# Kernel tuning notes

Measured on AMD Instinct MI355X. Metric: run time of the kernel, lower is better.

## Reference

```python
import jax, jax.numpy as jnp
import numpy as np

N_EMBEDDING = 32
HEAD_SIZE = 64
B, T = 8, 4096


def setup_inputs() -> dict:
    key = jax.random.key(0)
    kx, kk, kq, kv = jax.random.split(key, 4)
    x = jax.random.normal(kx, (B, T, N_EMBEDDING), dtype=jnp.float32)
    Wk = jax.random.normal(kk, (N_EMBEDDING, HEAD_SIZE), dtype=jnp.float32) * 0.05
    Wq = jax.random.normal(kq, (N_EMBEDDING, HEAD_SIZE), dtype=jnp.float32) * 0.05
    Wv = jax.random.normal(kv, (N_EMBEDDING, HEAD_SIZE), dtype=jnp.float32) * 0.05
    return {"x": x, "Wk": Wk, "Wq": Wq, "Wv": Wv}


def reference(x, Wk, Wq, Wv):
    # x: [B, T, C]; projections (no bias)
    k = jnp.einsum("btc,cd->btd", x, Wk)  # [B,T,D]
    q = jnp.einsum("btc,cd->btd", x, Wq)
    v = jnp.einsum("btc,cd->btd", x, Wv)
    # raw scores (NOTE: original module applies no 1/sqrt(D) scaling)
    wei = jnp.einsum("bqd,bkd->bqk", q, k)  # [B,T,T]
    t = x.shape[1]
    causal = jnp.tril(jnp.ones((t, t), dtype=bool))
    wei = jnp.where(causal[None, :, :], wei, -jnp.inf)
    wei = jax.nn.softmax(wei, axis=-1)
    out = jnp.einsum("bqk,bkd->bqd", wei, v)  # [B,T,D]
    return out
```

## Files before the change

kernel.cpp:

```cpp
#include <hip/hip_runtime.h>
#include <hip/hip_bf16.h>

constexpr int Bc = 8;
constexpr int Tt = 4096;
constexpr int Dd = 64;

typedef __attribute__((ext_vector_type(8))) short short8;
typedef __attribute__((ext_vector_type(4))) float floatx4;
typedef __attribute__((ext_vector_type(4))) __fp16 half4;
typedef __attribute__((ext_vector_type(2))) __fp16 half2v;
typedef uint4   __attribute__((may_alias)) uint4_a;
typedef short8  __attribute__((may_alias)) short8_a;
typedef ushort4 __attribute__((may_alias)) ushort4_a;
typedef float4  __attribute__((may_alias)) float4_a;
typedef half4   __attribute__((may_alias)) half4_a;

#define MFMA16(A, B, C)  __builtin_amdgcn_mfma_f32_16x16x32_bf16(A, B, C, 0, 0, 0)
#define MFMAH16(A, B, C) __builtin_amdgcn_mfma_f32_16x16x16f16(A, B, C, 0, 0, 0)
constexpr float LOG2E = 1.4426950408889634f;

__device__ __forceinline__ unsigned rnd16(float x) {
    unsigned u; __builtin_memcpy(&u, &x, 4); return u + 0x8000u;
}
__device__ __forceinline__ unsigned pk_bf2(float lo, float hi) {
    return __builtin_amdgcn_perm(rnd16(hi), rnd16(lo), 0x07060302);
}
__device__ __forceinline__ ushort4 pack4(floatx4 d) {
    union { unsigned u[2]; ushort4 v; } r;
    r.u[0] = pk_bf2(d[0], d[1]);
    r.u[1] = pk_bf2(d[2], d[3]);
    return r.v;
}
__device__ __forceinline__ short8 cvt8(float4 a, float4 b) {
    union { unsigned u[4]; short8 s; } r;
    r.u[0] = pk_bf2(a.x, a.y);
    r.u[1] = pk_bf2(a.z, a.w);
    r.u[2] = pk_bf2(b.x, b.y);
    r.u[3] = pk_bf2(b.z, b.w);
    return r.s;
}

__global__ __launch_bounds__(1024, 4) void attn_kernel(
    const float* __restrict__ x,
    const float* __restrict__ Wk, const float* __restrict__ Wq,
    const float* __restrict__ Wv,
    float* __restrict__ out)
{
    __shared__ uint4 sStage[4096];
    __shared__ uint4 sP[256];
    __shared__ uint4 sG[128];

    int b  = blockIdx.x & 7;
    int pr = blockIdx.x >> 3;
    int tid  = threadIdx.x;
    int wave = tid >> 6, lane = tid & 63;
    int group = wave >> 2, gw = wave & 3;
    int ln15 = lane & 15, quad = lane >> 4;
    size_t bT = (size_t)b * Tt;

    const int tg = tid & 255;
    const int srow = tg >> 2, scg = tg & 3;

    if (wave == 0) {
        floatx4 gC[2][2];
        #pragma unroll
        for (int mt = 0; mt < 2; ++mt)
            #pragma unroll
            for (int nt = 0; nt < 2; ++nt) gC[mt][nt] = (floatx4){0.f,0.f,0.f,0.f};
        #pragma unroll
        for (int kt = 0; kt < 2; ++kt) {
            short8 aG[2], bG[2];
            #pragma unroll
            for (int mt = 0; mt < 2; ++mt) {
                const float* qp = Wq + (ln15 + 16*mt)*64 + 32*kt + quad*8;
                float4 a = ((const float4_a*)qp)[0], bb = ((const float4_a*)qp)[1];
                a.x*=LOG2E; a.y*=LOG2E; a.z*=LOG2E; a.w*=LOG2E;
                bb.x*=LOG2E; bb.y*=LOG2E; bb.z*=LOG2E; bb.w*=LOG2E;
                aG[mt] = cvt8(a, bb);
                const float* kp = Wk + (ln15 + 16*mt)*64 + 32*kt + quad*8;
                bG[mt] = cvt8(((const float4_a*)kp)[0], ((const float4_a*)kp)[1]);
            }
            #pragma unroll
            for (int mt = 0; mt < 2; ++mt)
                #pragma unroll
                for (int nt = 0; nt < 2; ++nt)
                    gC[mt][nt] = MFMA16(aG[mt], bG[nt], gC[mt][nt]);
        }
        unsigned short* sGh = (unsigned short*)sG;
        #pragma unroll
        for (int mt = 0; mt < 2; ++mt)
            #pragma unroll
            for (int nt = 0; nt < 2; ++nt)
                *(ushort4_a*)(sGh + (16*nt + ln15)*32 + 16*mt + quad*4)
                    = pack4(gC[mt][nt]);
    }
    __syncthreads();

    const int gBase = group * 1024;
    unsigned short* sYh = (unsigned short*)sP;

    for (int phase = 0; phase < 2; ++phase) {
        const int qtP = phase ? pr : 63 - pr;
        const int q0 = qtP * 64;
        const int qrow = q0 + gw*16 + ln15;

        float4 pX0, pX1;
        if (group <= qtP) {
            const float* xp = x + (bT + group*64 + srow)*32 + scg*8;
            pX0 = ((const float4_a*)xp)[0];
            pX1 = ((const float4_a*)xp)[1];
        }

        if (wave < 8) {
            int qs = wave & 3, mt = wave >> 2;
            union { uint4 u; short8 s; } g;
            g.u = sG[(16*mt + ln15)*4 + quad];
            const float* xp = x + (bT + q0 + qs*16 + ln15)*32 + quad*8;
            short8 xq = cvt8(((const float4_a*)xp)[0], ((const float4_a*)xp)[1]);
            floatx4 d = (floatx4){0.f,0.f,0.f,0.f};
            d = MFMA16(g.s, xq, d);
            *(ushort4_a*)(sYh + (qs*16 + ln15)*32 + 16*mt + quad*4) = pack4(d);
        }
        __syncthreads();
        short8 bq;
        {
            union { uint4 u; short8 s; } t0;
            t0.u = sP[(gw*16 + ln15)*4 + quad];
            bq = t0.s;
        }

        floatx4 z4[2];
        z4[0] = (floatx4){0.f,0.f,0.f,0.f};
        z4[1] = (floatx4){0.f,0.f,0.f,0.f};
        float l_lane = 0.f;

        const int nIter = (qtP + 4) >> 2;

        for (int it = 0; it < nIter; ++it) {
            int kt = 4*it + group;
            bool active = (kt <= qtP);
            const int stB = gBase + (it & 1) * 512;
            if (active) {
                unsigned u0 = pk_bf2(pX0.x, pX0.y), u1 = pk_bf2(pX0.z, pX0.w);
                unsigned u2 = pk_bf2(pX1.x, pX1.y), u3 = pk_bf2(pX1.z, pX1.w);
                uint4 xu; xu.x = u0; xu.y = u1; xu.z = u2; xu.w = u3;
                sStage[stB + srow*4 + (scg ^ (srow & 3))] = xu;
                union { half2v h; unsigned short us[2]; } w01, w23, w45, w67;
                w01.h = __builtin_amdgcn_cvt_pkrtz(pX0.x, pX0.y);
                w23.h = __builtin_amdgcn_cvt_pkrtz(pX0.z, pX0.w);
                w45.h = __builtin_amdgcn_cvt_pkrtz(pX1.x, pX1.y);
                w67.h = __builtin_amdgcn_cvt_pkrtz(pX1.z, pX1.w);
                unsigned short hv[8] = { w01.us[0], w01.us[1], w23.us[0], w23.us[1],
                                         w45.us[0], w45.us[1], w67.us[0], w67.us[1] };
                unsigned short* sXh = (unsigned short*)(sStage + stB + 256);
                const int cb = scg * 8, gx = srow >> 2, ko = srow & 3;
                #pragma unroll
                for (int jj = 0; jj < 8; ++jj) {
                    int c = cb + jj;
                    sXh[c*64 + ((gx ^ (c & 15)) << 2) + ko] = hv[jj];
                }
            }
            __syncthreads();
            int ktn = kt + 4;
            if (ktn <= qtP) {
                const float* xp = x + (bT + ktn*64 + srow)*32 + scg*8;
                pX0 = ((const float4_a*)xp)[0];
                pX1 = ((const float4_a*)xp)[1];
            }
            if (!active) continue;
            int k0 = kt * 64;

            const int xsw = quad ^ (ln15 & 3);
            floatx4 s4[4];
            #pragma unroll
            for (int t = 0; t < 4; ++t) {
                union { uint4 u; short8 s; } a;
                a.u = sStage[stB + (16*t + ln15)*4 + xsw];
                floatx4 c = (floatx4){0.f,0.f,0.f,0.f};
                c = MFMA16(a.s, bq, c);
                s4[t] = c;
            }

            if (kt == qtP) {
                #pragma unroll
                for (int t = 0; t < 4; ++t) {
                    int keyb = k0 + 16*t + quad*4;
                    #pragma unroll
                    for (int r = 0; r < 4; ++r) {
                        float p = (keyb + r <= qrow) ? __builtin_amdgcn_exp2f(s4[t][r]) : 0.f;
                        s4[t][r] = p;
                        l_lane += p;
                    }
                }
            } else {
                #pragma unroll
                for (int t = 0; t < 4; ++t)
                    #pragma unroll
                    for (int r = 0; r < 4; ++r) {
                        float p = __builtin_amdgcn_exp2f(s4[t][r]);
                        s4[t][r] = p;
                        l_lane += p;
                    }
            }

            const unsigned short* sXh = (const unsigned short*)(sStage + stB + 256);
            #pragma unroll
            for (int t = 0; t < 4; ++t) {
                union { half2v h2[2]; half4 h4; } pb;
                pb.h2[0] = __builtin_amdgcn_cvt_pkrtz(s4[t][0], s4[t][1]);
                pb.h2[1] = __builtin_amdgcn_cvt_pkrtz(s4[t][2], s4[t][3]);
                const int gph = ((4*t + quad) ^ ln15) << 2;
                #pragma unroll
                for (int mt = 0; mt < 2; ++mt) {
                    half4 xa = *(const half4_a*)(sXh + (16*mt + ln15)*64 + gph);
                    z4[mt] = MFMAH16(xa, pb.h4, z4[mt]);
                }
            }
        }

        __syncthreads();
        int li = gw*64 + lane;
        ((float*)sP)[wave*64 + lane] = l_lane;
        if (group != 0) {
            float4* st = (float4*)(sStage + group*1024);
            st[li*2 + 0] = make_float4(z4[0][0], z4[0][1], z4[0][2], z4[0][3]);
            st[li*2 + 1] = make_float4(z4[1][0], z4[1][1], z4[1][2], z4[1][3]);
        }
        __syncthreads();
        if (group == 0) {
            short8 wv_f[4];
            #pragma unroll
            for (int t = 0; t < 4; ++t) {
                int col = 16*t + ln15;
                union { unsigned u[4]; short8 s; } rv;
                #pragma unroll
                for (int jj = 0; jj < 4; ++jj) {
                    const float* v0 = Wv + (quad*8 + 2*jj) * 64 + col;
                    rv.u[jj] = pk_bf2(v0[0], v0[64]);
                }
                wv_f[t] = rv.s;
            }
            float l = l_lane + ((float*)sP)[256 + li]
                    + ((float*)sP)[512 + li] + ((float*)sP)[768 + li];
            l += __shfl_xor(l, 16);
            l += __shfl_xor(l, 32);
            float inv = 1.f / l;
            #pragma unroll
            for (int g = 1; g < 4; ++g) {
                float4* st = (float4*)(sStage + g*1024);
                float4 a = st[li*2 + 0], bb = st[li*2 + 1];
                z4[0][0]+=a.x; z4[0][1]+=a.y; z4[0][2]+=a.z; z4[0][3]+=a.w;
                z4[1][0]+=bb.x; z4[1][1]+=bb.y; z4[1][2]+=bb.z; z4[1][3]+=bb.w;
            }
            unsigned short* sZb = (unsigned short*)sStage;
            #pragma unroll
            for (int mt = 0; mt < 2; ++mt)
                *(ushort4_a*)(sZb + (gw*16 + ln15)*32 + 16*mt + quad*4) = pack4(z4[mt]);
            union { uint4 u; short8 s; } zb;
            zb.u = sStage[(gw*16 + ln15)*4 + quad];
            #pragma unroll
            for (int t = 0; t < 4; ++t) {
                floatx4 o = (floatx4){0.f,0.f,0.f,0.f};
                o = MFMA16(wv_f[t], zb.s, o);
                *(float4_a*)(out + (bT + q0 + gw*16 + ln15)*Dd + 16*t + quad*4)
                    = make_float4(o[0]*inv, o[1]*inv, o[2]*inv, o[3]*inv);
            }
        }
        __syncthreads();
    }
}

extern "C" void kernel_launch(void* const* d_in, const int* in_sizes, int n_in,
                              void* d_out, int out_size, void* d_ws, size_t ws_size,
                              hipStream_t stream)
{
    const float* x  = (const float*)d_in[0];
    const float* Wk = (const float*)d_in[1];
    const float* Wq = (const float*)d_in[2];
    const float* Wv = (const float*)d_in[3];
    float* out = (float*)d_out;

    attn_kernel<<<Bc * 32, 1024, 0, stream>>>(x, Wk, Wq, Wv, out);
}
```

Measured before the change: 87.46 us.

## Split into prep kernel precomputing bf16/fp16 x layouts, then barrier-free attention

```diff
diff --git a/kernel.cpp b/kernel.cpp
--- a/kernel.cpp
+++ b/kernel.cpp
@@ -19,6 +19,11 @@
 #define MFMAH16(A, B, C) __builtin_amdgcn_mfma_f32_16x16x16f16(A, B, C, 0, 0, 0)
 constexpr float LOG2E = 1.4426950408889634f;
 
+constexpr size_t XB_OFF = 0;
+constexpr size_t YB_OFF = (size_t)2 << 20;
+constexpr size_t XT_OFF = (size_t)4 << 20;
+constexpr size_t WV_OFF = (size_t)6 << 20;
+
 __device__ __forceinline__ unsigned rnd16(float x) {
     unsigned u; __builtin_memcpy(&u, &x, 4); return u + 0x8000u;
 }
@@ -40,26 +45,29 @@
     return r.s;
 }
 
-__global__ __launch_bounds__(1024, 4) void attn_kernel(
+__global__ __launch_bounds__(256) void prep_kernel(
     const float* __restrict__ x,
     const float* __restrict__ Wk, const float* __restrict__ Wq,
     const float* __restrict__ Wv,
-    float* __restrict__ out)
+    char* __restrict__ ws)
 {
-    __shared__ uint4 sStage[4096];
-    __shared__ uint4 sP[256];
     __shared__ uint4 sG[128];
-
-    int b  = blockIdx.x & 7;
-    int pr = blockIdx.x >> 3;
-    int tid  = threadIdx.x;
-    int wave = tid >> 6, lane = tid & 63;
-    int group = wave >> 2, gw = wave & 3;
-    int ln15 = lane & 15, quad = lane >> 4;
-    size_t bT = (size_t)b * Tt;
-
-    const int tg = tid & 255;
-    const int srow = tg >> 2, scg = tg & 3;
+    __shared__ float sX[2048];
+
+    const int bi = blockIdx.x;
+    const int b = bi >> 6, ch = bi & 63;
+    const int tid = threadIdx.x;
+    const int wave = tid >> 6, lane = tid & 63;
+    const int ln15 = lane & 15, quad = lane >> 4;
+    const size_t bT = (size_t)b * Tt;
+    const int r0 = ch * 64;
+
+    const int lr = wave * 16 + ln15;
+    const float* xp = x + (bT + r0 + lr) * 32 + quad * 8;
+    float4 pX0 = ((const float4_a*)xp)[0];
+    float4 pX1 = ((const float4_a*)xp)[1];
+    *(float4_a*)(&sX[lr * 32 + quad * 8])     = pX0;
+    *(float4_a*)(&sX[lr * 32 + quad * 8 + 4]) = pX1;
 
     if (wave == 0) {
         floatx4 gC[2][2];
@@ -96,36 +104,85 @@
     }
     __syncthreads();
 
-    const int gBase = group * 1024;
-    unsigned short* sYh = (unsigned short*)sP;
-
-    for (int phase = 0; phase < 2; ++phase) {
-        const int qtP = phase ? pr : 63 - pr;
-        const int q0 = qtP * 64;
-        const int qrow = q0 + gw*16 + ln15;
-
-        float4 pX0, pX1;
-        if (group <= qtP) {
-            const float* xp = x + (bT + group*64 + srow)*32 + scg*8;
-            pX0 = ((const float4_a*)xp)[0];
-            pX1 = ((const float4_a*)xp)[1];
-        }
-
-        if (wave < 8) {
-            int qs = wave & 3, mt = wave >> 2;
+    union { unsigned u[4]; uint4 v; } xu;
+    xu.u[0] = pk_bf2(pX0.x, pX0.y); xu.u[1] = pk_bf2(pX0.z, pX0.w);
+    xu.u[2] = pk_bf2(pX1.x, pX1.y); xu.u[3] = pk_bf2(pX1.z, pX1.w);
+    *(uint4_a*)(ws + XB_OFF + (size_t)(bT + r0 + lr) * 64 + quad * 16) = xu.v;
+
+    {
+        short8 xq = cvt8(pX0, pX1);
+        unsigned short* yb = (unsigned short*)(ws + YB_OFF);
+        #pragma unroll
+        for (int mt = 0; mt < 2; ++mt) {
             union { uint4 u; short8 s; } g;
             g.u = sG[(16*mt + ln15)*4 + quad];
-            const float* xp = x + (bT + q0 + qs*16 + ln15)*32 + quad*8;
-            short8 xq = cvt8(((const float4_a*)xp)[0], ((const float4_a*)xp)[1]);
             floatx4 d = (floatx4){0.f,0.f,0.f,0.f};
             d = MFMA16(g.s, xq, d);
-            *(ushort4_a*)(sYh + (qs*16 + ln15)*32 + 16*mt + quad*4) = pack4(d);
-        }
-        __syncthreads();
+            *(ushort4_a*)(yb + (size_t)(bT + r0 + lr) * 32 + 16*mt + quad*4)
+                = pack4(d);
+        }
+    }
+
+    {
+        const int kc = tid >> 6;
+        const int c = (tid >> 1) & 31, kh = tid & 1;
+        float v[8];
+        #pragma unroll
+        for (int j = 0; j < 8; ++j) v[j] = sX[(kc*16 + kh*8 + j)*32 + c];
+        union { unsigned u[4]; uint4 q; } x4;
+        #pragma unroll
+        for (int j = 0; j < 4; ++j) {
+            union { half2v h; unsigned u; } p;
+            p.h = __builtin_amdgcn_cvt_pkrtz(v[2*j], v[2*j+1]);
+            x4.u[j] = p.u;
+        }
+        *(uint4_a*)(ws + XT_OFF
+                    + ((size_t)((b*256 + ch*4 + kc) * 32 + c)) * 32 + kh * 16)
+            = x4.q;
+    }
+
+    if (bi == 0 && wave == 2) {
+        const int d = lane;
+        unsigned short* wvb = (unsigned short*)(ws + WV_OFF);
+        float v[32];
+        #pragma unroll
+        for (int c2 = 0; c2 < 32; ++c2) v[c2] = Wv[c2*64 + d];
+        #pragma unroll
+        for (int i2 = 0; i2 < 16; ++i2)
+            ((unsigned*)(wvb + d*32))[i2] = pk_bf2(v[2*i2], v[2*i2+1]);
+    }
+}
+
+__global__ __launch_bounds__(1024, 4) void attn_kernel(
+    const char* __restrict__ ws, float* __restrict__ out)
+{
+    __shared__ float sZ[3 * 2048];
+    __shared__ float sL[3 * 256];
+    __shared__ uint4 sB[256];
+
+    const int b  = blockIdx.x & 7;
+    const int pr = blockIdx.x >> 3;
+    const int tid = threadIdx.x;
+    const int wave = tid >> 6, lane = tid & 63;
+    const int kg = wave >> 2, gw = wave & 3;
+    const int ln15 = lane & 15, quad = lane >> 4;
+    const size_t bT = (size_t)b * Tt;
+
+    const char* xbB = ws + XB_OFF + bT * 64;
+    const char* xtB = ws + XT_OFF + (size_t)b * (256 * 1024);
+    const int aOff = ln15 * 64 + quad * 16;
+    const int xOff = ln15 * 32 + quad * 8;
+
+    for (int phase = 0; phase < 2; ++phase) {
+        const int qt = phase ? pr : 63 - pr;
+        const int q0 = qt * 64;
+        const int qrow = q0 + gw * 16 + ln15;
+
         short8 bq;
         {
             union { uint4 u; short8 s; } t0;
-            t0.u = sP[(gw*16 + ln15)*4 + quad];
+            t0.u = *(const uint4_a*)(ws + YB_OFF + (size_t)(bT + qrow) * 64
+                                     + quad * 16);
             bq = t0.s;
         }
 
@@ -134,62 +191,38 @@
         z4[1] = (floatx4){0.f,0.f,0.f,0.f};
         float l_lane = 0.f;
 
-        const int nIter = (qtP + 4) >> 2;
-
-        for (int it = 0; it < nIter; ++it) {
-            int kt = 4*it + group;
-            bool active = (kt <= qtP);
-            const int stB = gBase + (it & 1) * 512;
-            if (active) {
-                unsigned u0 = pk_bf2(pX0.x, pX0.y), u1 = pk_bf2(pX0.z, pX0.w);
-                unsigned u2 = pk_bf2(pX1.x, pX1.y), u3 = pk_bf2(pX1.z, pX1.w);
-                uint4 xu; xu.x = u0; xu.y = u1; xu.z = u2; xu.w = u3;
-                sStage[stB + srow*4 + (scg ^ (srow & 3))] = xu;
-                union { half2v h; unsigned short us[2]; } w01, w23, w45, w67;
-                w01.h = __builtin_amdgcn_cvt_pkrtz(pX0.x, pX0.y);
-                w23.h = __builtin_amdgcn_cvt_pkrtz(pX0.z, pX0.w);
-                w45.h = __builtin_amdgcn_cvt_pkrtz(pX1.x, pX1.y);
-                w67.h = __builtin_amdgcn_cvt_pkrtz(pX1.z, pX1.w);
-                unsigned short hv[8] = { w01.us[0], w01.us[1], w23.us[0], w23.us[1],
-                                         w45.us[0], w45.us[1], w67.us[0], w67.us[1] };
-                unsigned short* sXh = (unsigned short*)(sStage + stB + 256);
-                const int cb = scg * 8, gx = srow >> 2, ko = srow & 3;
-                #pragma unroll
-                for (int jj = 0; jj < 8; ++jj) {
-                    int c = cb + jj;
-                    sXh[c*64 + ((gx ^ (c & 15)) << 2) + ko] = hv[jj];
-                }
-            }
-            __syncthreads();
-            int ktn = kt + 4;
-            if (ktn <= qtP) {
-                const float* xp = x + (bT + ktn*64 + srow)*32 + scg*8;
-                pX0 = ((const float4_a*)xp)[0];
-                pX1 = ((const float4_a*)xp)[1];
-            }
-            if (!active) continue;
-            int k0 = kt * 64;
-
-            const int xsw = quad ^ (ln15 & 3);
+        short8 aA[4], aB4[4];
+
+        auto LDA = [&](int k, short8* a) {
+            const char* p = xbB + (size_t)k * 4096 + aOff;
+            #pragma unroll
+            for (int t = 0; t < 4; ++t)
+                a[t] = *(const short8_a*)(p + t * 1024);
+        };
+
+        auto BODY = [&](int kt, const short8* a) {
+            const char* px = xtB + (size_t)kt * 4096 + xOff;
+            half4 xa[8];
+            #pragma unroll
+            for (int t = 0; t < 4; ++t) {
+                xa[2*t]   = *(const half4_a*)(px + t * 1024);
+                xa[2*t+1] = *(const half4_a*)(px + t * 1024 + 512);
+            }
             floatx4 s4[4];
             #pragma unroll
             for (int t = 0; t < 4; ++t) {
-                union { uint4 u; short8 s; } a;
-                a.u = sStage[stB + (16*t + ln15)*4 + xsw];
-                floatx4 c = (floatx4){0.f,0.f,0.f,0.f};
-                c = MFMA16(a.s, bq, c);
-                s4[t] = c;
-            }
-
-            if (kt == qtP) {
+                floatx4 c0 = (floatx4){0.f,0.f,0.f,0.f};
+                s4[t] = MFMA16(a[t], bq, c0);
+            }
+            if (kt == qt) {
                 #pragma unroll
                 for (int t = 0; t < 4; ++t) {
-                    int keyb = k0 + 16*t + quad*4;
+                    const int keyb = kt*64 + 16*t + quad*4;
                     #pragma unroll
                     for (int r = 0; r < 4; ++r) {
-                        float p = (keyb + r <= qrow) ? __builtin_amdgcn_exp2f(s4[t][r]) : 0.f;
-                        s4[t][r] = p;
-                        l_lane += p;
+                        float p = (keyb + r <= qrow)
+                                  ? __builtin_amdgcn_exp2f(s4[t][r]) : 0.f;
+                        s4[t][r] = p; l_lane += p;
                     }
                 }
             } else {
@@ -198,71 +231,76 @@
                     #pragma unroll
                     for (int r = 0; r < 4; ++r) {
                         float p = __builtin_amdgcn_exp2f(s4[t][r]);
-                        s4[t][r] = p;
-                        l_lane += p;
+                        s4[t][r] = p; l_lane += p;
                     }
             }
-
-            const unsigned short* sXh = (const unsigned short*)(sStage + stB + 256);
             #pragma unroll
             for (int t = 0; t < 4; ++t) {
                 union { half2v h2[2]; half4 h4; } pb;
                 pb.h2[0] = __builtin_amdgcn_cvt_pkrtz(s4[t][0], s4[t][1]);
                 pb.h2[1] = __builtin_amdgcn_cvt_pkrtz(s4[t][2], s4[t][3]);
-                const int gph = ((4*t + quad) ^ ln15) << 2;
-                #pragma unroll
-                for (int mt = 0; mt < 2; ++mt) {
-                    half4 xa = *(const half4_a*)(sXh + (16*mt + ln15)*64 + gph);
-                    z4[mt] = MFMAH16(xa, pb.h4, z4[mt]);
-                }
+                z4[0] = MFMAH16(xa[2*t],   pb.h4, z4[0]);
+                z4[1] = MFMAH16(xa[2*t+1], pb.h4, z4[1]);
+            }
+        };
+
+        int kt = kg;
+        if (kt <= qt) {
+            LDA(kt, aA);
+            while (true) {
+                int kn = kt + 4;
+                LDA(kn <= qt ? kn : kt, aB4);
+                BODY(kt, aA);
+                if (kn > qt) break;
+                kt = kn; kn = kt + 4;
+                LDA(kn <= qt ? kn : kt, aA);
+                BODY(kt, aB4);
+                if (kn > qt) break;
+                kt = kn;
             }
         }
 
         __syncthreads();
-        int li = gw*64 + lane;
-        ((float*)sP)[wave*64 + lane] = l_lane;
-        if (group != 0) {
-            float4* st = (float4*)(sStage + group*1024);
-            st[li*2 + 0] = make_float4(z4[0][0], z4[0][1], z4[0][2], z4[0][3]);
-            st[li*2 + 1] = make_float4(z4[1][0], z4[1][1], z4[1][2], z4[1][3]);
+        const int li = gw * 64 + lane;
+        if (kg != 0) {
+            sL[(kg - 1) * 256 + li] = l_lane;
+            float4* zp = (float4*)(sZ + (kg - 1) * 2048);
+            zp[li*2 + 0] = make_float4(z4[0][0], z4[0][1], z4[0][2], z4[0][3]);
+            zp[li*2 + 1] = make_float4(z4[1][0], z4[1][1], z4[1][2], z4[1][3]);
         }
         __syncthreads();
-        if (group == 0) {
-            short8 wv_f[4];
-            #pragma unroll
-            for (int t = 0; t < 4; ++t) {
-                int col = 16*t + ln15;
-                union { unsigned u[4]; short8 s; } rv;
-                #pragma unroll
-                for (int jj = 0; jj < 4; ++jj) {
-                    const float* v0 = Wv + (quad*8 + 2*jj) * 64 + col;
-                    rv.u[jj] = pk_bf2(v0[0], v0[64]);
-                }
-                wv_f[t] = rv.s;
-            }
-            float l = l_lane + ((float*)sP)[256 + li]
-                    + ((float*)sP)[512 + li] + ((float*)sP)[768 + li];
+        if (kg == 0) {
+            float l = l_lane + sL[li] + sL[256 + li] + sL[512 + li];
+            #pragma unroll
+            for (int g = 0; g < 3; ++g) {
+                const float4* zp = (const float4*)(sZ + g * 2048);
+                float4 za = zp[li*2 + 0], zb2 = zp[li*2 + 1];
+                z4[0][0]+=za.x;  z4[0][1]+=za.y;  z4[0][2]+=za.z;  z4[0][3]+=za.w;
+                z4[1][0]+=zb2.x; z4[1][1]+=zb2.y; z4[1][2]+=zb2.z; z4[1][3]+=zb2.w;
+            }
             l += __shfl_xor(l, 16);
             l += __shfl_xor(l, 32);
-            float inv = 1.f / l;
-            #pragma unroll
-            for (int g = 1; g < 4; ++g) {
-                float4* st = (float4*)(sStage + g*1024);
-                float4 a = st[li*2 + 0], bb = st[li*2 + 1];
-                z4[0][0]+=a.x; z4[0][1]+=a.y; z4[0][2]+=a.z; z4[0][3]+=a.w;
-                z4[1][0]+=bb.x; z4[1][1]+=bb.y; z4[1][2]+=bb.z; z4[1][3]+=bb.w;
-            }
-            unsigned short* sZb = (unsigned short*)sStage;
+            const float inv = 1.f / l;
+            const unsigned short* wvb = (const unsigned short*)(ws + WV_OFF);
+            short8 wv_f[4];
+            #pragma unroll
+            for (int t = 0; t < 4; ++t) {
+                union { uint4 u; short8 s; } w0;
+                w0.u = *(const uint4_a*)(wvb + (16*t + ln15) * 32 + quad * 8);
+                wv_f[t] = w0.s;
+            }
+            unsigned short* sZb = (unsigned short*)sB;
             #pragma unroll
             for (int mt = 0; mt < 2; ++mt)
-                *(ushort4_a*)(sZb + (gw*16 + ln15)*32 + 16*mt + quad*4) = pack4(z4[mt]);
+                *(ushort4_a*)(sZb + (gw*16 + ln15)*32 + 16*mt + quad*4)
+                    = pack4(z4[mt]);
             union { uint4 u; short8 s; } zb;
-            zb.u = sStage[(gw*16 + ln15)*4 + quad];
+            zb.u = sB[(gw*16 + ln15)*4 + quad];
             #pragma unroll
             for (int t = 0; t < 4; ++t) {
                 floatx4 o = (floatx4){0.f,0.f,0.f,0.f};
                 o = MFMA16(wv_f[t], zb.s, o);
-                *(float4_a*)(out + (bT + q0 + gw*16 + ln15)*Dd + 16*t + quad*4)
+                *(float4_a*)(out + (bT + (size_t)qrow) * Dd + 16*t + quad*4)
                     = make_float4(o[0]*inv, o[1]*inv, o[2]*inv, o[3]*inv);
             }
         }
@@ -280,5 +318,6 @@
     const float* Wv = (const float*)d_in[3];
     float* out = (float*)d_out;
 
-    attn_kernel<<<Bc * 32, 1024, 0, stream>>>(x, Wk, Wq, Wv, out);
-}
+    prep_kernel<<<512, 256, 0, stream>>>(x, Wk, Wq, Wv, (char*)d_ws);
+    attn_kernel<<<Bc * 32, 1024, 0, stream>>>((const char*)d_ws, out);
+}
```

After: 101.0 us. 15.5% more time.
